# Kernel optimization log

Measured on AMD Instinct MI355X. Metric: run time of the kernel, lower is better.

The kernel has to match this reference:

```python
import jax, jax.numpy as jnp
import numpy as np

N = 50000   # nodes
E = 800000  # edges (avg degree 16)
D = 96      # input feature dim
U = 96      # units (== D, so no dense_i projection)


def _glorot(key, fan_in, fan_out):
    limit = np.sqrt(6.0 / (fan_in + fan_out)).astype(np.float32)
    return jax.random.uniform(key, (fan_in, fan_out), jnp.float32, -limit, limit)


def setup_inputs() -> dict:
    key = jax.random.key(0)
    ks = jax.random.split(key, 8)
    X = jax.random.normal(ks[0], (N, D), jnp.float32)
    row = jax.random.randint(ks[1], (E,), 0, N, jnp.int32)   # destination nodes
    col = jax.random.randint(ks[2], (E,), 0, N, jnp.int32)   # source nodes
    a_vals = jax.random.uniform(ks[3], (E,), jnp.float32)    # adjacency values
    return {
        "X": X,
        "a_vals": a_vals,
        "Wn": _glorot(ks[4], D, U), "bn": jnp.zeros((U,), jnp.float32),
        "Wgi": _glorot(ks[5], D, U), "bgi": jnp.zeros((U,), jnp.float32),
        "Wgn": _glorot(ks[6], U, U), "bgn": jnp.zeros((U,), jnp.float32),
        "row": row, "col": col,
    }


def reference(X, a_vals, Wn, bn, Wgi, bgi, Wgn, bgn, row, col):
    # new_X = dense_n(X); new_X = A @ new_X  (SpMM via gather + segment_sum)
    newX = X @ Wn + bn                       # [N, U]
    msgs = a_vals[:, None] * newX[col]       # [E, U]
    agg = jax.ops.segment_sum(msgs, row, num_segments=N)  # [N, U]
    # gate = sigmoid(dense_gate_i(X) + dense_gate_n(agg))
    gate = jax.nn.sigmoid(X @ Wgi + bgi + agg @ Wgn + bgn)
    # units == inp_dim -> no dense_i; gated residual combine
    return agg * gate + X * (1.0 - gate)
```

## Files before the change

### kernel.cpp

```cpp
#include <hip/hip_runtime.h>
#include <math.h>


#define DU 96
#define DU4 24
#define NSUB 64
#define NGRP 8
#define HMAX 6656
#define CAPG_PAD 16384

typedef unsigned int uint;
typedef unsigned short ushort;
typedef __attribute__((ext_vector_type(8))) short short8;
typedef __attribute__((ext_vector_type(4))) float f32x4;

__device__ inline uint bf16r(float x) {
  uint u = __float_as_uint(x);
  return (u + 0x7FFFu + ((u >> 16) & 1u)) >> 16;
}

__global__ __launch_bounds__(256) void k_fuse1(
    const float* __restrict__ X, const float* __restrict__ Wn,
    const float* __restrict__ bn, const float* __restrict__ Wgi,
    const float* __restrict__ Wgn, const int* __restrict__ row,
    ushort* __restrict__ Xb, ushort* __restrict__ newXb,
    ushort* __restrict__ WTgi, ushort* __restrict__ WTgn,
    ushort* __restrict__ pc, int N, int E, int ntile) {
  __shared__ __align__(16) char smem[31744];
  ushort* WL = (ushort*)smem;
  typedef ushort XsRow[104];
  XsRow* Xs = (XsRow*)(smem + 18432);
  const int tid = threadIdx.x;
  const int lane = tid & 63, w = tid >> 6;
  const int m = lane & 15, q = lane >> 4;

  if ((int)blockIdx.x < ntile) {
    if (blockIdx.x == 0) {
      for (int i = tid; i < DU * DU; i += 256) {
        int n = i / DU, k = i % DU;
        WTgi[i] = (ushort)bf16r(Wgi[k * DU + n]);
      }
    } else if (blockIdx.x == 1) {
      for (int i = tid; i < DU * DU; i += 256) {
        int n = i / DU, k = i % DU;
        WTgn[i] = (ushort)bf16r(Wgn[k * DU + n]);
      }
    }
    for (int idx = tid; idx < 9216; idx += 256) {
      int j = idx & 7, ln = (idx >> 3) & 63, tk = idx >> 9;
      int ks = tk / 6, t = tk % 6;
      int k = ks * 32 + (ln >> 4) * 8 + j;
      int n = t * 16 + (ln & 15);
      WL[idx] = (ushort)bf16r(Wn[k * DU + n]);
    }
    const int row0 = blockIdx.x * 64;
    for (int i = tid; i < 64 * 48; i += 256) {
      int r = i / 48, cu = i % 48;
      int gr = row0 + r;
      uint packed = 0;
      if (gr < N) {
        float2 v = ((const float2*)X)[(size_t)gr * 48 + cu];
        packed = bf16r(v.x) | (bf16r(v.y) << 16);
        ((uint*)Xb)[(size_t)gr * 48 + cu] = packed;
      }
      *(uint*)&Xs[r][cu * 2] = packed;
    }
    __syncthreads();

    f32x4 acc[6];
#pragma unroll
    for (int t = 0; t < 6; ++t) acc[t] = (f32x4){0.f, 0.f, 0.f, 0.f};
#pragma unroll
    for (int ks = 0; ks < 3; ++ks) {
      short8 af = *(const short8*)&Xs[w * 16 + m][ks * 32 + q * 8];
#pragma unroll
      for (int t = 0; t < 6; ++t) {
        short8 bf = *(const short8*)&WL[((ks * 6 + t) * 64 + lane) * 8];
        acc[t] = __builtin_amdgcn_mfma_f32_16x16x32_bf16(af, bf, acc[t], 0, 0, 0);
      }
    }
    __syncthreads();
#pragma unroll
    for (int t = 0; t < 6; ++t) {
      int c = t * 16 + m;
      float bb = bn[c];
#pragma unroll
      for (int i = 0; i < 4; ++i)
        Xs[w * 16 + q * 4 + i][c] = (ushort)bf16r(acc[t][i] + bb);
    }
    __syncthreads();
    for (int i = tid; i < 64 * 48; i += 256) {
      int r = i / 48, cu = i % 48;
      int gr = row0 + r;
      if (gr < N) ((uint*)newXb)[(size_t)gr * 48 + cu] = *(uint*)&Xs[r][cu * 2];
    }
  } else {
    int* hist = (int*)smem;
    const int hb = (int)blockIdx.x - ntile;
    const int g = (int)(blockIdx.x & 7);
    const int sub = hb >> 3;
    const int d0 = (int)((long long)N * g >> 3);
    const int d1 = (int)((long long)N * (g + 1) >> 3);
    const int hs = d1 - d0;
    for (int j = tid; j < hs; j += 256) hist[j] = 0;
    __syncthreads();
    const int e0 = (int)(((long long)E * sub) / NSUB);
    const int e1 = (int)(((long long)E * (sub + 1)) / NSUB);
    int i = e0 + tid;
    for (; i + 1792 < e1; i += 2048) {
      int a0 = row[i], a1 = row[i + 256], a2 = row[i + 512], a3 = row[i + 768];
      int a4 = row[i + 1024], a5 = row[i + 1280], a6 = row[i + 1536], a7 = row[i + 1792];
      if (a0 >= d0 && a0 < d1) atomicAdd(&hist[a0 - d0], 1);
      if (a1 >= d0 && a1 < d1) atomicAdd(&hist[a1 - d0], 1);
      if (a2 >= d0 && a2 < d1) atomicAdd(&hist[a2 - d0], 1);
      if (a3 >= d0 && a3 < d1) atomicAdd(&hist[a3 - d0], 1);
      if (a4 >= d0 && a4 < d1) atomicAdd(&hist[a4 - d0], 1);
      if (a5 >= d0 && a5 < d1) atomicAdd(&hist[a5 - d0], 1);
      if (a6 >= d0 && a6 < d1) atomicAdd(&hist[a6 - d0], 1);
      if (a7 >= d0 && a7 < d1) atomicAdd(&hist[a7 - d0], 1);
    }
    for (; i < e1; i += 256) {
      int d = row[i];
      if (d >= d0 && d < d1) atomicAdd(&hist[d - d0], 1);
    }
    __syncthreads();
    for (int j = tid; j < hs; j += 256) pc[(size_t)sub * N + d0 + j] = (ushort)hist[j];
  }
}

__global__ __launch_bounds__(256) void k_colsum(const ushort* __restrict__ pc,
                                                ushort* __restrict__ psub,
                                                ushort* __restrict__ deg, int N) {
  int d2 = (blockIdx.x * 256 + threadIdx.x) * 2;
  if (d2 >= N) return;
  int runLo = 0, runHi = 0;
#pragma unroll 8
  for (int s = 0; s < NSUB; ++s) {
    uint v = *(const uint*)(pc + (size_t)s * N + d2);
    *(uint*)(psub + (size_t)s * N + d2) = (uint)runLo | ((uint)runHi << 16);
    runLo += (int)(v & 0xFFFFu);
    runHi += (int)(v >> 16);
  }
  *(uint*)(deg + d2) = (uint)runLo | ((uint)runHi << 16);
}

__global__ __launch_bounds__(1024) void k_off(const ushort* __restrict__ deg,
                                              int* __restrict__ off,
                                              int N, int E) {
  __shared__ int ws[16];
  const int g = blockIdx.x;
  const int tid = threadIdx.x;
  const int lane = tid & 63, wid = tid >> 6;
  const int d0 = (int)((long long)N * g >> 3);
  const int d1 = (int)((long long)N * (g + 1) >> 3);
  const int hs = d1 - d0;
  const int PT = 8;
  const int j0 = tid * PT;
  int v[PT];
  int s = 0;
#pragma unroll
  for (int k = 0; k < PT; ++k) {
    int j = j0 + k;
    v[k] = (j < hs) ? (int)deg[d0 + j] : 0;
    s += v[k];
  }
  int incl = s;
#pragma unroll
  for (int dlt = 1; dlt < 64; dlt <<= 1) {
    int t = __shfl_up(incl, dlt, 64);
    if (lane >= dlt) incl += t;
  }
  if (lane == 63) ws[wid] = incl;
  __syncthreads();
  int wexcl = 0;
#pragma unroll
  for (int k = 0; k < 16; ++k)
    if (k < wid) wexcl += ws[k];
  const int capg = (E >> 3) + CAPG_PAD;
  int running = g * capg + wexcl + (incl - s);
#pragma unroll
  for (int k = 0; k < PT; ++k) {
    int j = j0 + k;
    if (j < hs) { off[d0 + j] = running; running += v[k]; }
  }
}

__global__ __launch_bounds__(512) void k_scatter(const int* __restrict__ row,
                                                 const int* __restrict__ col,
                                                 const float* __restrict__ a_vals,
                                                 const int* __restrict__ off,
                                                 const ushort* __restrict__ psub,
                                                 int2* __restrict__ ec,
                                                 int N, int E) {
  __shared__ int cur[HMAX];
  const int g = (int)(blockIdx.x & 7);
  const int sub = (int)(blockIdx.x >> 3);
  const int d0 = (int)((long long)N * g >> 3);
  const int d1 = (int)((long long)N * (g + 1) >> 3);
  const int hs = d1 - d0;
  for (int j = threadIdx.x; j < hs; j += 512)
    cur[j] = off[d0 + j] + (int)psub[(size_t)sub * N + d0 + j];
  __syncthreads();
  const int e0 = (int)(((long long)E * sub) / NSUB);
  const int e1 = (int)(((long long)E * (sub + 1)) / NSUB);
  int i = e0 + (int)threadIdx.x;
  for (; i + 3584 < e1; i += 4096) {
    int a0 = row[i], a1 = row[i + 512], a2 = row[i + 1024], a3 = row[i + 1536];
    int a4 = row[i + 2048], a5 = row[i + 2560], a6 = row[i + 3072], a7 = row[i + 3584];
    if (a0 >= d0 && a0 < d1) {
      int s = atomicAdd(&cur[a0 - d0], 1);
      ec[s] = make_int2(col[i], __float_as_int(a_vals[i]));
    }
    if (a1 >= d0 && a1 < d1) {
      int s = atomicAdd(&cur[a1 - d0], 1);
      ec[s] = make_int2(col[i + 512], __float_as_int(a_vals[i + 512]));
    }
    if (a2 >= d0 && a2 < d1) {
      int s = atomicAdd(&cur[a2 - d0], 1);
      ec[s] = make_int2(col[i + 1024], __float_as_int(a_vals[i + 1024]));
    }
    if (a3 >= d0 && a3 < d1) {
      int s = atomicAdd(&cur[a3 - d0], 1);
      ec[s] = make_int2(col[i + 1536], __float_as_int(a_vals[i + 1536]));
    }
    if (a4 >= d0 && a4 < d1) {
      int s = atomicAdd(&cur[a4 - d0], 1);
      ec[s] = make_int2(col[i + 2048], __float_as_int(a_vals[i + 2048]));
    }
    if (a5 >= d0 && a5 < d1) {
      int s = atomicAdd(&cur[a5 - d0], 1);
      ec[s] = make_int2(col[i + 2560], __float_as_int(a_vals[i + 2560]));
    }
    if (a6 >= d0 && a6 < d1) {
      int s = atomicAdd(&cur[a6 - d0], 1);
      ec[s] = make_int2(col[i + 3072], __float_as_int(a_vals[i + 3072]));
    }
    if (a7 >= d0 && a7 < d1) {
      int s = atomicAdd(&cur[a7 - d0], 1);
      ec[s] = make_int2(col[i + 3584], __float_as_int(a_vals[i + 3584]));
    }
  }
  for (; i < e1; i += 512) {
    int d = row[i];
    if (d >= d0 && d < d1) {
      int s = atomicAdd(&cur[d - d0], 1);
      ec[s] = make_int2(col[i], __float_as_int(a_vals[i]));
    }
  }
}

__global__ __launch_bounds__(512, 6) void k_aggGate(
    const ushort* __restrict__ Xb, const ushort* __restrict__ newXb,
    const int* __restrict__ off, const ushort* __restrict__ deg,
    const int2* __restrict__ ec, const ushort* __restrict__ WTgi,
    const ushort* __restrict__ WTgn, const float* __restrict__ bgi,
    const float* __restrict__ bgn, const float* __restrict__ X,
    float* __restrict__ Out, int N) {
  __shared__ ushort As[64][104];
  __shared__ float Gs[64][100];
  const int tid = threadIdx.x;
  const int lane = tid & 63, w = tid >> 6;
  const int m = lane & 15, q = lane >> 4;
  const int row0 = (int)blockIdx.x * 64;

#define GCN_FMA8(ACC, V, A)                                      \
  ACC[0] = fmaf(A, __uint_as_float(V.x << 16), ACC[0]);          \
  ACC[1] = fmaf(A, __uint_as_float(V.x & 0xFFFF0000u), ACC[1]);  \
  ACC[2] = fmaf(A, __uint_as_float(V.y << 16), ACC[2]);          \
  ACC[3] = fmaf(A, __uint_as_float(V.y & 0xFFFF0000u), ACC[3]);  \
  ACC[4] = fmaf(A, __uint_as_float(V.z << 16), ACC[4]);          \
  ACC[5] = fmaf(A, __uint_as_float(V.z & 0xFFFF0000u), ACC[5]);  \
  ACC[6] = fmaf(A, __uint_as_float(V.w << 16), ACC[6]);          \
  ACC[7] = fmaf(A, __uint_as_float(V.w & 0xFFFF0000u), ACC[7])
  for (int t = tid; t < 64 * 12; t += 512) {
    const int rl = t / 12, c = t % 12;
    const int r = row0 + rl;
    float accA[8], accB[8];
#pragma unroll
    for (int k = 0; k < 8; ++k) { accA[k] = 0.f; accB[k] = 0.f; }
    if (r < N) {
      const int2* ep = ec + off[r];
      const int e1 = (int)deg[r];
      int e = 0;
      for (; e + 8 <= e1; e += 8) {
        int2 p0 = ep[e + 0];
        int2 p1 = ep[e + 1];
        int2 p2 = ep[e + 2];
        int2 p3 = ep[e + 3];
        int2 p4 = ep[e + 4];
        int2 p5 = ep[e + 5];
        int2 p6 = ep[e + 6];
        int2 p7 = ep[e + 7];
        uint4 v0 = *(const uint4*)(newXb + (size_t)p0.x * DU + c * 8);
        uint4 v1 = *(const uint4*)(newXb + (size_t)p1.x * DU + c * 8);
        uint4 v2 = *(const uint4*)(newXb + (size_t)p2.x * DU + c * 8);
        uint4 v3 = *(const uint4*)(newXb + (size_t)p3.x * DU + c * 8);
        uint4 v4 = *(const uint4*)(newXb + (size_t)p4.x * DU + c * 8);
        uint4 v5 = *(const uint4*)(newXb + (size_t)p5.x * DU + c * 8);
        uint4 v6 = *(const uint4*)(newXb + (size_t)p6.x * DU + c * 8);
        uint4 v7 = *(const uint4*)(newXb + (size_t)p7.x * DU + c * 8);
        float a0 = __int_as_float(p0.y), a1 = __int_as_float(p1.y);
        float a2 = __int_as_float(p2.y), a3 = __int_as_float(p3.y);
        float a4 = __int_as_float(p4.y), a5 = __int_as_float(p5.y);
        float a6 = __int_as_float(p6.y), a7 = __int_as_float(p7.y);
        GCN_FMA8(accA, v0, a0);
        GCN_FMA8(accB, v1, a1);
        GCN_FMA8(accA, v2, a2);
        GCN_FMA8(accB, v3, a3);
        GCN_FMA8(accA, v4, a4);
        GCN_FMA8(accB, v5, a5);
        GCN_FMA8(accA, v6, a6);
        GCN_FMA8(accB, v7, a7);
      }
      for (; e + 4 <= e1; e += 4) {
        int2 p0 = ep[e + 0];
        int2 p1 = ep[e + 1];
        int2 p2 = ep[e + 2];
        int2 p3 = ep[e + 3];
        uint4 v0 = *(const uint4*)(newXb + (size_t)p0.x * DU + c * 8);
        uint4 v1 = *(const uint4*)(newXb + (size_t)p1.x * DU + c * 8);
        uint4 v2 = *(const uint4*)(newXb + (size_t)p2.x * DU + c * 8);
        uint4 v3 = *(const uint4*)(newXb + (size_t)p3.x * DU + c * 8);
        float a0 = __int_as_float(p0.y), a1 = __int_as_float(p1.y);
        float a2 = __int_as_float(p2.y), a3 = __int_as_float(p3.y);
        GCN_FMA8(accA, v0, a0);
        GCN_FMA8(accB, v1, a1);
        GCN_FMA8(accA, v2, a2);
        GCN_FMA8(accB, v3, a3);
      }
      for (; e < e1; ++e) {
        int2 p = ep[e];
        uint4 v = *(const uint4*)(newXb + (size_t)p.x * DU + c * 8);
        float a = __int_as_float(p.y);
        GCN_FMA8(accA, v, a);
      }
    }
#pragma unroll
    for (int k = 0; k < 8; ++k) accA[k] += accB[k];
    uint4 o;
    o.x = bf16r(accA[0]) | (bf16r(accA[1]) << 16);
    o.y = bf16r(accA[2]) | (bf16r(accA[3]) << 16);
    o.z = bf16r(accA[4]) | (bf16r(accA[5]) << 16);
    o.w = bf16r(accA[6]) | (bf16r(accA[7]) << 16);
    *(uint4*)&As[rl][c * 8] = o;
  }
#undef GCN_FMA8
  __syncthreads();

  const int rq = w >> 1, th = w & 1;
  int ar = row0 + rq * 16 + m;
  if (ar > N - 1) ar = N - 1;
  f32x4 acc[3];
#pragma unroll
  for (int t = 0; t < 3; ++t) acc[t] = (f32x4){0.f, 0.f, 0.f, 0.f};
#pragma unroll
  for (int ks = 0; ks < 3; ++ks) {
    short8 af = *(const short8*)(Xb + (size_t)ar * DU + ks * 32 + q * 8);
    short8 ag = *(const short8*)&As[rq * 16 + m][ks * 32 + q * 8];
#pragma unroll
    for (int t = 0; t < 3; ++t) {
      const int ct = th * 3 + t;
      short8 bf = *(const short8*)(WTgi + (size_t)(ct * 16 + m) * DU + ks * 32 + q * 8);
      acc[t] = __builtin_amdgcn_mfma_f32_16x16x32_bf16(af, bf, acc[t], 0, 0, 0);
      short8 bg = *(const short8*)(WTgn + (size_t)(ct * 16 + m) * DU + ks * 32 + q * 8);
      acc[t] = __builtin_amdgcn_mfma_f32_16x16x32_bf16(ag, bg, acc[t], 0, 0, 0);
    }
  }
#pragma unroll
  for (int t = 0; t < 3; ++t) {
    const int c = (th * 3 + t) * 16 + m;
    const float bb = bgi[c] + bgn[c];
#pragma unroll
    for (int i = 0; i < 4; ++i) {
      float z = acc[t][i] + bb;
      Gs[rq * 16 + q * 4 + i][c] = 1.f / (1.f + __expf(-z));
    }
  }
  __syncthreads();

  for (int j = tid; j < 64 * DU4; j += 512) {
    int r = j / DU4, c = j % DU4;
    int gr = row0 + r;
    if (gr < N) {
      float4 xv = ((const float4*)X)[(size_t)gr * DU4 + c];
      uint2 av = *(const uint2*)&As[r][c * 4];
      float a0 = __uint_as_float(av.x << 16);
      float a1 = __uint_as_float(av.x & 0xFFFF0000u);
      float a2 = __uint_as_float(av.y << 16);
      float a3 = __uint_as_float(av.y & 0xFFFF0000u);
      const float* gp = &Gs[r][c * 4];
      float4 o;
      o.x = xv.x + gp[0] * (a0 - xv.x);
      o.y = xv.y + gp[1] * (a1 - xv.y);
      o.z = xv.z + gp[2] * (a2 - xv.z);
      o.w = xv.w + gp[3] * (a3 - xv.w);
      ((float4*)Out)[(size_t)gr * DU4 + c] = o;
    }
  }
}

extern "C" void kernel_launch(void* const* d_in, const int* in_sizes, int n_in,
                              void* d_out, int out_size, void* d_ws, size_t ws_size,
                              hipStream_t stream) {
  const float* X      = (const float*)d_in[0];
  const float* a_vals = (const float*)d_in[1];
  const float* Wn     = (const float*)d_in[2];
  const float* bn     = (const float*)d_in[3];
  const float* Wgi    = (const float*)d_in[4];
  const float* bgi    = (const float*)d_in[5];
  const float* Wgn    = (const float*)d_in[6];
  const float* bgn    = (const float*)d_in[7];
  const int*   row    = (const int*)d_in[8];
  const int*   col    = (const int*)d_in[9];
  float* out = (float*)d_out;

  const int N = in_sizes[0] / DU;
  const int E = in_sizes[1];
  const int ntile = (N + 63) / 64;
  const int G1 = ntile + NSUB * NGRP;
  const int capg = (E >> 3) + CAPG_PAD;

  int2*   ec    = (int2*)d_ws;
  ushort* Xb    = (ushort*)(ec + (size_t)NGRP * capg);
  ushort* newXb = Xb + (size_t)N * DU;
  ushort* WTgi  = newXb + (size_t)N * DU;
  ushort* WTgn  = WTgi + DU * DU;
  int*    off   = (int*)(WTgn + DU * DU);
  ushort* deg   = (ushort*)(off + ((N + 3) & ~3));
  ushort* pc    = deg + (((size_t)N + 7) & ~7ull);
  ushort* psub  = pc + (size_t)NSUB * N;

  k_fuse1  <<<G1, 256, 0, stream>>>(X, Wn, bn, Wgi, Wgn, row,
                                    Xb, newXb, WTgi, WTgn, pc, N, E, ntile);
  k_colsum <<<(N / 2 + 255) / 256, 256, 0, stream>>>(pc, psub, deg, N);
  k_off    <<<NGRP, 1024, 0, stream>>>(deg, off, N, E);
  k_scatter<<<NSUB * NGRP, 512, 0, stream>>>(row, col, a_vals, off, psub, ec, N, E);
  k_aggGate<<<ntile, 512, 0, stream>>>(Xb, newXb, off, deg, ec, WTgi, WTgn,
                                       bgi, bgn, X, out, N);
}
```

Before: 211.9 us.

## Shrink aggGate blocks to 256 threads with per-thread row ownership

The aggregation/gate kernel now runs 256 threads per block. Each group of 4 threads owns one destination row and loops over 3 column chunks, so the row's offset and degree are loaded once and reused. The previous version mapped 768 (row, chunk) tasks over 512 threads, which left half the threads idle on the second pass. The gate MFMA stage now has each of the 4 waves compute all 6 column tiles for its 16 rows instead of splitting columns across wave pairs. The cost is three sequential edge-list passes per thread and higher register use per thread, which may lower occupancy.

```diff
diff --git a/kernel.cpp b/kernel.cpp
--- a/kernel.cpp
+++ b/kernel.cpp
@@ -249,7 +249,7 @@
   }
 }
 
-__global__ __launch_bounds__(512, 6) void k_aggGate(
+__global__ __launch_bounds__(256) void k_aggGate(
     const ushort* __restrict__ Xb, const ushort* __restrict__ newXb,
     const int* __restrict__ off, const ushort* __restrict__ deg,
     const int2* __restrict__ ec, const ushort* __restrict__ WTgi,
@@ -263,6 +263,11 @@
   const int m = lane & 15, q = lane >> 4;
   const int row0 = (int)blockIdx.x * 64;
 
+  const int rl = tid >> 2;
+  const int r = row0 + rl;
+  const int2* ep = nullptr;
+  int ecnt = 0;
+  if (r < N) { ep = ec + off[r]; ecnt = (int)deg[r]; }
 #define GCN_FMA8(ACC, V, A)                                      \
   ACC[0] = fmaf(A, __uint_as_float(V.x << 16), ACC[0]);          \
   ACC[1] = fmaf(A, __uint_as_float(V.x & 0xFFFF0000u), ACC[1]);  \
@@ -272,68 +277,64 @@
   ACC[5] = fmaf(A, __uint_as_float(V.z & 0xFFFF0000u), ACC[5]);  \
   ACC[6] = fmaf(A, __uint_as_float(V.w << 16), ACC[6]);          \
   ACC[7] = fmaf(A, __uint_as_float(V.w & 0xFFFF0000u), ACC[7])
-  for (int t = tid; t < 64 * 12; t += 512) {
-    const int rl = t / 12, c = t % 12;
-    const int r = row0 + rl;
+#pragma unroll
+  for (int p = 0; p < 3; ++p) {
+    const int c = p * 4 + (tid & 3);
     float accA[8], accB[8];
 #pragma unroll
     for (int k = 0; k < 8; ++k) { accA[k] = 0.f; accB[k] = 0.f; }
-    if (r < N) {
-      const int2* ep = ec + off[r];
-      const int e1 = (int)deg[r];
-      int e = 0;
-      for (; e + 8 <= e1; e += 8) {
-        int2 p0 = ep[e + 0];
-        int2 p1 = ep[e + 1];
-        int2 p2 = ep[e + 2];
-        int2 p3 = ep[e + 3];
-        int2 p4 = ep[e + 4];
-        int2 p5 = ep[e + 5];
-        int2 p6 = ep[e + 6];
-        int2 p7 = ep[e + 7];
-        uint4 v0 = *(const uint4*)(newXb + (size_t)p0.x * DU + c * 8);
-        uint4 v1 = *(const uint4*)(newXb + (size_t)p1.x * DU + c * 8);
-        uint4 v2 = *(const uint4*)(newXb + (size_t)p2.x * DU + c * 8);
-        uint4 v3 = *(const uint4*)(newXb + (size_t)p3.x * DU + c * 8);
-        uint4 v4 = *(const uint4*)(newXb + (size_t)p4.x * DU + c * 8);
-        uint4 v5 = *(const uint4*)(newXb + (size_t)p5.x * DU + c * 8);
-        uint4 v6 = *(const uint4*)(newXb + (size_t)p6.x * DU + c * 8);
-        uint4 v7 = *(const uint4*)(newXb + (size_t)p7.x * DU + c * 8);
-        float a0 = __int_as_float(p0.y), a1 = __int_as_float(p1.y);
-        float a2 = __int_as_float(p2.y), a3 = __int_as_float(p3.y);
-        float a4 = __int_as_float(p4.y), a5 = __int_as_float(p5.y);
-        float a6 = __int_as_float(p6.y), a7 = __int_as_float(p7.y);
-        GCN_FMA8(accA, v0, a0);
-        GCN_FMA8(accB, v1, a1);
-        GCN_FMA8(accA, v2, a2);
-        GCN_FMA8(accB, v3, a3);
-        GCN_FMA8(accA, v4, a4);
-        GCN_FMA8(accB, v5, a5);
-        GCN_FMA8(accA, v6, a6);
-        GCN_FMA8(accB, v7, a7);
-      }
-      for (; e + 4 <= e1; e += 4) {
-        int2 p0 = ep[e + 0];
-        int2 p1 = ep[e + 1];
-        int2 p2 = ep[e + 2];
-        int2 p3 = ep[e + 3];
-        uint4 v0 = *(const uint4*)(newXb + (size_t)p0.x * DU + c * 8);
-        uint4 v1 = *(const uint4*)(newXb + (size_t)p1.x * DU + c * 8);
-        uint4 v2 = *(const uint4*)(newXb + (size_t)p2.x * DU + c * 8);
-        uint4 v3 = *(const uint4*)(newXb + (size_t)p3.x * DU + c * 8);
-        float a0 = __int_as_float(p0.y), a1 = __int_as_float(p1.y);
-        float a2 = __int_as_float(p2.y), a3 = __int_as_float(p3.y);
-        GCN_FMA8(accA, v0, a0);
-        GCN_FMA8(accB, v1, a1);
-        GCN_FMA8(accA, v2, a2);
-        GCN_FMA8(accB, v3, a3);
-      }
-      for (; e < e1; ++e) {
-        int2 p = ep[e];
-        uint4 v = *(const uint4*)(newXb + (size_t)p.x * DU + c * 8);
-        float a = __int_as_float(p.y);
-        GCN_FMA8(accA, v, a);
-      }
+    int e = 0;
+    for (; e + 8 <= ecnt; e += 8) {
+      int2 p0 = ep[e + 0];
+      int2 p1 = ep[e + 1];
+      int2 p2 = ep[e + 2];
+      int2 p3 = ep[e + 3];
+      int2 p4 = ep[e + 4];
+      int2 p5 = ep[e + 5];
+      int2 p6 = ep[e + 6];
+      int2 p7 = ep[e + 7];
+      uint4 v0 = *(const uint4*)(newXb + (size_t)p0.x * DU + c * 8);
+      uint4 v1 = *(const uint4*)(newXb + (size_t)p1.x * DU + c * 8);
+      uint4 v2 = *(const uint4*)(newXb + (size_t)p2.x * DU + c * 8);
+      uint4 v3 = *(const uint4*)(newXb + (size_t)p3.x * DU + c * 8);
+      uint4 v4 = *(const uint4*)(newXb + (size_t)p4.x * DU + c * 8);
+      uint4 v5 = *(const uint4*)(newXb + (size_t)p5.x * DU + c * 8);
+      uint4 v6 = *(const uint4*)(newXb + (size_t)p6.x * DU + c * 8);
+      uint4 v7 = *(const uint4*)(newXb + (size_t)p7.x * DU + c * 8);
+      float a0 = __int_as_float(p0.y), a1 = __int_as_float(p1.y);
+      float a2 = __int_as_float(p2.y), a3 = __int_as_float(p3.y);
+      float a4 = __int_as_float(p4.y), a5 = __int_as_float(p5.y);
+      float a6 = __int_as_float(p6.y), a7 = __int_as_float(p7.y);
+      GCN_FMA8(accA, v0, a0);
+      GCN_FMA8(accB, v1, a1);
+      GCN_FMA8(accA, v2, a2);
+      GCN_FMA8(accB, v3, a3);
+      GCN_FMA8(accA, v4, a4);
+      GCN_FMA8(accB, v5, a5);
+      GCN_FMA8(accA, v6, a6);
+      GCN_FMA8(accB, v7, a7);
+    }
+    for (; e + 4 <= ecnt; e += 4) {
+      int2 p0 = ep[e + 0];
+      int2 p1 = ep[e + 1];
+      int2 p2 = ep[e + 2];
+      int2 p3 = ep[e + 3];
+      uint4 v0 = *(const uint4*)(newXb + (size_t)p0.x * DU + c * 8);
+      uint4 v1 = *(const uint4*)(newXb + (size_t)p1.x * DU + c * 8);
+      uint4 v2 = *(const uint4*)(newXb + (size_t)p2.x * DU + c * 8);
+      uint4 v3 = *(const uint4*)(newXb + (size_t)p3.x * DU + c * 8);
+      float a0 = __int_as_float(p0.y), a1 = __int_as_float(p1.y);
+      float a2 = __int_as_float(p2.y), a3 = __int_as_float(p3.y);
+      GCN_FMA8(accA, v0, a0);
+      GCN_FMA8(accB, v1, a1);
+      GCN_FMA8(accA, v2, a2);
+      GCN_FMA8(accB, v3, a3);
+    }
+    for (; e < ecnt; ++e) {
+      int2 pp = ep[e];
+      uint4 v = *(const uint4*)(newXb + (size_t)pp.x * DU + c * 8);
+      float a = __int_as_float(pp.y);
+      GCN_FMA8(accA, v, a);
     }
 #pragma unroll
     for (int k = 0; k < 8; ++k) accA[k] += accB[k];
@@ -347,48 +348,46 @@
 #undef GCN_FMA8
   __syncthreads();
 
-  const int rq = w >> 1, th = w & 1;
-  int ar = row0 + rq * 16 + m;
+  int ar = row0 + w * 16 + m;
   if (ar > N - 1) ar = N - 1;
-  f32x4 acc[3];
-#pragma unroll
-  for (int t = 0; t < 3; ++t) acc[t] = (f32x4){0.f, 0.f, 0.f, 0.f};
+  f32x4 acc[6];
+#pragma unroll
+  for (int t = 0; t < 6; ++t) acc[t] = (f32x4){0.f, 0.f, 0.f, 0.f};
 #pragma unroll
   for (int ks = 0; ks < 3; ++ks) {
     short8 af = *(const short8*)(Xb + (size_t)ar * DU + ks * 32 + q * 8);
-    short8 ag = *(const short8*)&As[rq * 16 + m][ks * 32 + q * 8];
-#pragma unroll
-    for (int t = 0; t < 3; ++t) {
-      const int ct = th * 3 + t;
-      short8 bf = *(const short8*)(WTgi + (size_t)(ct * 16 + m) * DU + ks * 32 + q * 8);
+    short8 ag = *(const short8*)&As[w * 16 + m][ks * 32 + q * 8];
+#pragma unroll
+    for (int t = 0; t < 6; ++t) {
+      short8 bf = *(const short8*)(WTgi + (size_t)(t * 16 + m) * DU + ks * 32 + q * 8);
       acc[t] = __builtin_amdgcn_mfma_f32_16x16x32_bf16(af, bf, acc[t], 0, 0, 0);
-      short8 bg = *(const short8*)(WTgn + (size_t)(ct * 16 + m) * DU + ks * 32 + q * 8);
+      short8 bg = *(const short8*)(WTgn + (size_t)(t * 16 + m) * DU + ks * 32 + q * 8);
       acc[t] = __builtin_amdgcn_mfma_f32_16x16x32_bf16(ag, bg, acc[t], 0, 0, 0);
     }
   }
 #pragma unroll
-  for (int t = 0; t < 3; ++t) {
-    const int c = (th * 3 + t) * 16 + m;
+  for (int t = 0; t < 6; ++t) {
+    const int c = t * 16 + m;
     const float bb = bgi[c] + bgn[c];
 #pragma unroll
     for (int i = 0; i < 4; ++i) {
       float z = acc[t][i] + bb;
-      Gs[rq * 16 + q * 4 + i][c] = 1.f / (1.f + __expf(-z));
+      Gs[w * 16 + q * 4 + i][c] = 1.f / (1.f + __expf(-z));
     }
   }
   __syncthreads();
 
-  for (int j = tid; j < 64 * DU4; j += 512) {
-    int r = j / DU4, c = j % DU4;
-    int gr = row0 + r;
+  for (int j = tid; j < 64 * DU4; j += 256) {
+    int r2 = j / DU4, c = j % DU4;
+    int gr = row0 + r2;
     if (gr < N) {
       float4 xv = ((const float4*)X)[(size_t)gr * DU4 + c];
-      uint2 av = *(const uint2*)&As[r][c * 4];
+      uint2 av = *(const uint2*)&As[r2][c * 4];
       float a0 = __uint_as_float(av.x << 16);
       float a1 = __uint_as_float(av.x & 0xFFFF0000u);
       float a2 = __uint_as_float(av.y << 16);
       float a3 = __uint_as_float(av.y & 0xFFFF0000u);
-      const float* gp = &Gs[r][c * 4];
+      const float* gp = &Gs[r2][c * 4];
       float4 o;
       o.x = xv.x + gp[0] * (a0 - xv.x);
       o.y = xv.y + gp[1] * (a1 - xv.y);
@@ -435,6 +434,6 @@
   k_colsum <<<(N / 2 + 255) / 256, 256, 0, stream>>>(pc, psub, deg, N);
   k_off    <<<NGRP, 1024, 0, stream>>>(deg, off, N, E);
   k_scatter<<<NSUB * NGRP, 512, 0, stream>>>(row, col, a_vals, off, psub, ec, N, E);
-  k_aggGate<<<ntile, 512, 0, stream>>>(Xb, newXb, off, deg, ec, WTgi, WTgn,
+  k_aggGate<<<ntile, 256, 0, stream>>>(Xb, newXb, off, deg, ec, WTgi, WTgn,
                                        bgi, bgn, X, out, N);
 }
```

Measured after the change: 204.5 us. 3.5% less time.
